# Performance work log

Measured on AMD Instinct MI355X. Metric: run time of the kernel, lower is better.

Reference implementation:

```python
import jax, jax.numpy as jnp
import numpy as np

NUM_EMBEDDINGS = 2048
EMBEDDING_DIM = 128
BETA = 0.25


def setup_inputs() -> dict:
    key = jax.random.key(0)
    k1, k2 = jax.random.split(key)
    z = jax.random.normal(k1, (64, 32, 32, EMBEDDING_DIM), dtype=jnp.float32)
    # nn.Embedding init: uniform(-1/K, 1/K)
    emb = jax.random.uniform(k2, (NUM_EMBEDDINGS, EMBEDDING_DIM), dtype=jnp.float32,
                             minval=-1.0 / NUM_EMBEDDINGS, maxval=1.0 / NUM_EMBEDDINGS)
    return {"z": z, "emb": emb}


def reference(z, emb):
    beta = BETA
    flat = z.reshape(-1, EMBEDDING_DIM)  # [N, D]
    dist = (jnp.sum(flat * flat, axis=1, keepdims=True)
            - 2.0 * flat @ emb.T
            + jnp.sum(emb * emb, axis=1))
    indices = jnp.argmin(dist, axis=1)  # [N]
    quantized = emb[indices].reshape(z.shape)
    # commitment / codebook loss
    loss = (jnp.mean((jax.lax.stop_gradient(quantized) - z) ** 2)
            + beta * jnp.mean((quantized - jax.lax.stop_gradient(z)) ** 2))
    # straight-through estimator
    quantized_st = z + jax.lax.stop_gradient(quantized - z)
    indices_out = indices.reshape(z.shape[0], -1)
    return quantized_st, indices_out, loss
```

## Files before the change

### kernel.cpp

```cpp
#include <hip/hip_runtime.h>

#define NUM_EMB 2048
#define DIM     128
#define NVEC    65536
#define MARGIN  1.0e-3f
#define CAP     32
#define CHUNK   256
#define NCHUNK  (NUM_EMB / CHUNK)
#define ES      136
#define ZS      132

typedef float  f32x4 __attribute__((ext_vector_type(4)));
typedef short  s16x8 __attribute__((ext_vector_type(8)));

__device__ __forceinline__ ushort f2bf(float f) {
    unsigned u = __float_as_uint(f);
    u = (u + 0x7fffu + ((u >> 16) & 1u)) >> 16;
    return (ushort)u;
}

__device__ __forceinline__ float np_pairwise_sumsq_128(const float* __restrict__ p)
{
    float r[8];
    #pragma unroll
    for (int j = 0; j < 8; ++j) { float v = p[j]; r[j] = __fmul_rn(v, v); }
    #pragma unroll
    for (int i = 8; i < 128; i += 8)
        #pragma unroll
        for (int j = 0; j < 8; ++j) { float v = p[i + j]; r[j] = __fadd_rn(r[j], __fmul_rn(v, v)); }
    float s01 = __fadd_rn(r[0], r[1]);
    float s23 = __fadd_rn(r[2], r[3]);
    float s45 = __fadd_rn(r[4], r[5]);
    float s67 = __fadd_rn(r[6], r[7]);
    return __fadd_rn(__fadd_rn(s01, s23), __fadd_rn(s45, s67));
}

__device__ __forceinline__ float dot_seg(const float4* __restrict__ zp,
                                         const float4* __restrict__ ep,
                                         int seg, float dot)
{
    float4 e[8], zz[8];
    #pragma unroll
    for (int i = 0; i < 8; ++i) { e[i] = ep[seg * 8 + i]; zz[i] = zp[seg * 8 + i]; }
    #pragma unroll
    for (int i = 0; i < 8; ++i) {
        dot = fmaf(zz[i].x, e[i].x, dot);
        dot = fmaf(zz[i].y, e[i].y, dot);
        dot = fmaf(zz[i].z, e[i].z, dot);
        dot = fmaf(zz[i].w, e[i].w, dot);
    }
    return dot;
}

__global__ __launch_bounds__(256)
void prep_kernel(const float* __restrict__ emb,
                 float* __restrict__ enorm,
                 float* __restrict__ accum,
                 unsigned* __restrict__ cand_cnt,
                 ushort* __restrict__ emb_bf)
{
    int g = blockIdx.x * 256 + threadIdx.x;
    cand_cnt[g] = 0u;
    if (g == 0) *accum = 0.0f;

    float4 v = ((const float4*)emb)[g];
    ushort4 b;
    b.x = f2bf(v.x); b.y = f2bf(v.y); b.z = f2bf(v.z); b.w = f2bf(v.w);
    ((ushort4*)emb_bf)[g] = b;

    if (g < NUM_EMB)
        enorm[g] = np_pairwise_sumsq_128(emb + (size_t)g * DIM);
}

__global__ __launch_bounds__(256, 2)
void approx_kernel(const float* __restrict__ z,
                   const ushort* __restrict__ emb_bf,
                   const float* __restrict__ enorm,
                   unsigned* __restrict__ cand_cnt,
                   ushort* __restrict__ cand)
{
    __shared__ __align__(16) ushort eS[CHUNK * ES];
    __shared__ float cS[CHUNK];

    const int tid  = threadIdx.x;
    const int w    = tid >> 6;
    const int lane = tid & 63;
    const int col  = lane & 15;
    const int quad = lane >> 4;
    const int rowbase = blockIdx.x * 128 + w * 32;

    s16x8 afrag[2][4];
    #pragma unroll
    for (int rt = 0; rt < 2; ++rt) {
        const float* zr = z + (size_t)(rowbase + rt * 16 + col) * DIM;
        #pragma unroll
        for (int kt = 0; kt < 4; ++kt) {
            const float4* p = (const float4*)(zr + kt * 32 + quad * 8);
            float4 f0 = p[0], f1 = p[1];
            s16x8 a;
            a[0] = (short)f2bf(f0.x); a[1] = (short)f2bf(f0.y);
            a[2] = (short)f2bf(f0.z); a[3] = (short)f2bf(f0.w);
            a[4] = (short)f2bf(f1.x); a[5] = (short)f2bf(f1.y);
            a[6] = (short)f2bf(f1.z); a[7] = (short)f2bf(f1.w);
            afrag[rt][kt] = a;
        }
    }

    float minv[2][4], thr[2][4];
    #pragma unroll
    for (int rt = 0; rt < 2; ++rt)
        #pragma unroll
        for (int r = 0; r < 4; ++r) minv[rt][r] = 3.0e38f;

    for (int vis = 0; vis < 9; ++vis) {
        const int c = (vis == 0) ? 0 : (vis - 1);
        __syncthreads();
        const uint4* src = (const uint4*)(emb_bf + (size_t)c * CHUNK * DIM);
        #pragma unroll
        for (int i = 0; i < 16; ++i) {
            int li   = i * 256 + tid;
            int code = li >> 4, fc = li & 15;
            *(uint4*)&eS[code * ES + fc * 8] = src[li];
        }
        cS[tid] = enorm[c * CHUNK + tid];
        __syncthreads();

        #pragma unroll 4
        for (int t = 0; t < 16; ++t) {
            s16x8 bfrag[4];
            #pragma unroll
            for (int kt = 0; kt < 4; ++kt)
                bfrag[kt] = *(const s16x8*)&eS[(t * 16 + col) * ES + kt * 32 + quad * 8];

            f32x4 acc[2];
            #pragma unroll
            for (int rt = 0; rt < 2; ++rt) {
                f32x4 a = {0.0f, 0.0f, 0.0f, 0.0f};
                #pragma unroll
                for (int kt = 0; kt < 4; ++kt)
                    a = __builtin_amdgcn_mfma_f32_16x16x32_bf16(afrag[rt][kt], bfrag[kt], a, 0, 0, 0);
                acc[rt] = a;
            }

            float Cc     = cS[t * 16 + col];
            int   code_g = c * CHUNK + t * 16 + col;
            #pragma unroll
            for (int rt = 0; rt < 2; ++rt)
                #pragma unroll
                for (int r = 0; r < 4; ++r) {
                    float g = fmaf(-2.0f, acc[rt][r], Cc);
                    minv[rt][r] = fminf(minv[rt][r], g);
                    if (vis > 0 && g <= thr[rt][r]) {
                        int row_g = rowbase + rt * 16 + quad * 4 + r;
                        unsigned pos = atomicAdd(&cand_cnt[row_g], 1u);
                        if (pos < CAP) cand[(size_t)row_g * CAP + pos] = (ushort)code_g;
                    }
                }
        }

        #pragma unroll
        for (int rt = 0; rt < 2; ++rt)
            #pragma unroll
            for (int r = 0; r < 4; ++r) {
                float v = minv[rt][r];
                v = fminf(v, __shfl_xor(v, 1, 64));
                v = fminf(v, __shfl_xor(v, 2, 64));
                v = fminf(v, __shfl_xor(v, 4, 64));
                v = fminf(v, __shfl_xor(v, 8, 64));
                minv[rt][r] = v;
                thr[rt][r]  = v + MARGIN;
            }
    }
}

__global__ __launch_bounds__(256)
void rerank_kernel(const float* __restrict__ z,
                   const float* __restrict__ emb,
                   const float* __restrict__ enorm,
                   const unsigned* __restrict__ cand_cnt,
                   const ushort* __restrict__ cand,
                   float* __restrict__ out_q,
                   float* __restrict__ out_idx_f,
                   float* __restrict__ accum)
{
    __shared__ float zs[64 * ZS];
    __shared__ float As[64];
    __shared__ int   bidx[64];
    __shared__ int   ovf_list[64];
    __shared__ int   ovf_n;
    __shared__ float rv[4];
    __shared__ int   rvi[4];
    __shared__ float wsum[4];

    const int tid = threadIdx.x;
    const int m0  = blockIdx.x * 64;
    if (tid == 0) ovf_n = 0;

    #pragma unroll
    for (int i = 0; i < 8; ++i) {
        int li = tid + i * 256;
        int m  = li >> 5, dc = li & 31;
        float4 v = ((const float4*)(z + (size_t)(m0 + m) * DIM))[dc];
        *(float4*)&zs[m * ZS + dc * 4] = v;
    }
    __syncthreads();
    if (tid < 64) As[tid] = np_pairwise_sumsq_128(&zs[tid * ZS]);
    __syncthreads();

    const int row_l = tid >> 2;
    const int sub   = tid & 3;
    const int row_g = m0 + row_l;
    const unsigned cnt = cand_cnt[row_g];
    const float A = As[row_l];
    const float4* zp = (const float4*)&zs[row_l * ZS];

    float bv = 3.0e38f;
    int   bi = 0x7fffffff;

    if (cnt <= CAP) {
        for (unsigned ci = sub; ci < cnt; ci += 4) {
            int j = (int)cand[(size_t)row_g * CAP + ci];
            const float4* ep = (const float4*)(emb + (size_t)j * DIM);
            float dot = 0.0f;
            #pragma unroll
            for (int seg = 0; seg < 4; ++seg) dot = dot_seg(zp, ep, seg, dot);
            float t1 = fmaf(-2.0f, dot, A);
            float s  = __fadd_rn(t1, enorm[j]);
            if (s < bv || (s == bv && j < bi)) { bv = s; bi = j; }
        }
    }
    #pragma unroll
    for (int off = 1; off <= 2; off <<= 1) {
        float v  = __shfl_xor(bv, off, 64);
        int   ix = __shfl_xor(bi, off, 64);
        if (v < bv || (v == bv && ix < bi)) { bv = v; bi = ix; }
    }
    if (sub == 0) {
        if (cnt <= CAP) bidx[row_l] = bi;
        else { int p = atomicAdd(&ovf_n, 1); ovf_list[p] = row_l; }
    }
    __syncthreads();

    const int n_ovf = ovf_n;
    for (int o = 0; o < n_ovf; ++o) {
        const int rl = ovf_list[o];
        const float Ar = As[rl];
        const float4* zp2 = (const float4*)&zs[rl * ZS];
        float bv2 = 3.0e38f;
        int   bi2 = 0x7fffffff;
        for (int jj = 0; jj < 8; ++jj) {
            int j = tid * 8 + jj;
            const float4* ep = (const float4*)(emb + (size_t)j * DIM);
            float dot = 0.0f;
            #pragma unroll
            for (int seg = 0; seg < 4; ++seg) dot = dot_seg(zp2, ep, seg, dot);
            float t1 = fmaf(-2.0f, dot, Ar);
            float s  = __fadd_rn(t1, enorm[j]);
            if (s < bv2) { bv2 = s; bi2 = j; }
        }
        #pragma unroll
        for (int off = 1; off < 64; off <<= 1) {
            float v  = __shfl_xor(bv2, off, 64);
            int   ix = __shfl_xor(bi2, off, 64);
            if (v < bv2 || (v == bv2 && ix < bi2)) { bv2 = v; bi2 = ix; }
        }
        if ((tid & 63) == 0) { rv[tid >> 6] = bv2; rvi[tid >> 6] = bi2; }
        __syncthreads();
        if (tid == 0) {
            float fv = rv[0]; int fi = rvi[0];
            #pragma unroll
            for (int ww = 1; ww < 4; ++ww) {
                if (rv[ww] < fv || (rv[ww] == fv && rvi[ww] < fi)) { fv = rv[ww]; fi = rvi[ww]; }
            }
            bidx[rl] = fi;
        }
        __syncthreads();
    }

    if (tid < 64) out_idx_f[m0 + tid] = (float)bidx[tid];

    float part = 0.0f;
    #pragma unroll
    for (int i = 0; i < 8; ++i) {
        int li = tid + i * 256;
        int m  = li >> 5, dc = li & 31;
        int j  = bidx[m];
        float4 q  = ((const float4*)(emb + (size_t)j * DIM))[dc];
        float4 zv = *(const float4*)&zs[m * ZS + dc * 4];
        float4 o;
        o.x = __fadd_rn(zv.x, __fsub_rn(q.x, zv.x));
        o.y = __fadd_rn(zv.y, __fsub_rn(q.y, zv.y));
        o.z = __fadd_rn(zv.z, __fsub_rn(q.z, zv.z));
        o.w = __fadd_rn(zv.w, __fsub_rn(q.w, zv.w));
        ((float4*)out_q)[(size_t)(m0 + m) * 32 + dc] = o;
        float dx = q.x - zv.x, dy = q.y - zv.y, dz = q.z - zv.z, dw = q.w - zv.w;
        part += dx * dx + dy * dy + dz * dz + dw * dw;
    }
    #pragma unroll
    for (int off = 32; off > 0; off >>= 1)
        part += __shfl_down(part, off, 64);
    if ((tid & 63) == 0) wsum[tid >> 6] = part;
    __syncthreads();
    if (tid == 0) atomicAdd(accum, wsum[0] + wsum[1] + wsum[2] + wsum[3]);
}

__global__ void finalize_kernel(const float* __restrict__ accum,
                                float* __restrict__ out_loss)
{
    *out_loss = 1.25f * (*accum) / 8388608.0f;
}

extern "C" void kernel_launch(void* const* d_in, const int* in_sizes, int n_in,
                              void* d_out, int out_size, void* d_ws, size_t ws_size,
                              hipStream_t stream)
{
    const float* z   = (const float*)d_in[0];
    const float* emb = (const float*)d_in[1];
    float* out = (float*)d_out;

    char*     ws       = (char*)d_ws;
    float*    enorm    = (float*)ws;
    float*    accum    = (float*)(ws + 8192);
    unsigned* cand_cnt = (unsigned*)(ws + 16384);
    ushort*   cand     = (ushort*)(ws + 16384 + 262144);
    ushort*   emb_bf   = (ushort*)(ws + 16384 + 262144 + 4194304);

    prep_kernel   <<<NVEC / 256, 256, 0, stream>>>(emb, enorm, accum, cand_cnt, emb_bf);
    approx_kernel <<<512,        256, 0, stream>>>(z, emb_bf, enorm, cand_cnt, cand);
    rerank_kernel <<<NVEC / 64,  256, 0, stream>>>(z, emb, enorm, cand_cnt, cand,
                                                   out, out + 8388608, accum);
    finalize_kernel<<<1, 1, 0, stream>>>(accum, out + 8388608 + 65536);
}
```

Measured before the change: 275.7 us.

## Use 1024-thread approx blocks with one 16-row tile per wave

The approximate-distance kernel now runs 256 blocks of 16 waves instead of 512 blocks of 4 waves, and each wave owns 16 query rows rather than 32. The staged bf16 codebook chunk in shared memory is reused by four times as many waves, so L2-to-LDS traffic per query row drops. The cost is half as much MFMA work per B-fragment LDS read in each wave, which puts more pressure on LDS bandwidth, plus coarser blocks and heavier barrier synchronization.

Result: faster. 225.7 us (-18.1%).

```diff
diff --git a/kernel.cpp b/kernel.cpp
--- a/kernel.cpp
+++ b/kernel.cpp
@@ -72,7 +72,7 @@
         enorm[g] = np_pairwise_sumsq_128(emb + (size_t)g * DIM);
 }
 
-__global__ __launch_bounds__(256, 2)
+__global__ __launch_bounds__(1024, 1)
 void approx_kernel(const float* __restrict__ z,
                    const ushort* __restrict__ emb_bf,
                    const float* __restrict__ enorm,
@@ -87,12 +87,11 @@
     const int lane = tid & 63;
     const int col  = lane & 15;
     const int quad = lane >> 4;
-    const int rowbase = blockIdx.x * 128 + w * 32;
-
-    s16x8 afrag[2][4];
-    #pragma unroll
-    for (int rt = 0; rt < 2; ++rt) {
-        const float* zr = z + (size_t)(rowbase + rt * 16 + col) * DIM;
+    const int rowbase = blockIdx.x * 256 + w * 16;
+
+    s16x8 afrag[4];
+    {
+        const float* zr = z + (size_t)(rowbase + col) * DIM;
         #pragma unroll
         for (int kt = 0; kt < 4; ++kt) {
             const float4* p = (const float4*)(zr + kt * 32 + quad * 8);
@@ -102,27 +101,25 @@
             a[2] = (short)f2bf(f0.z); a[3] = (short)f2bf(f0.w);
             a[4] = (short)f2bf(f1.x); a[5] = (short)f2bf(f1.y);
             a[6] = (short)f2bf(f1.z); a[7] = (short)f2bf(f1.w);
-            afrag[rt][kt] = a;
-        }
-    }
-
-    float minv[2][4], thr[2][4];
-    #pragma unroll
-    for (int rt = 0; rt < 2; ++rt)
-        #pragma unroll
-        for (int r = 0; r < 4; ++r) minv[rt][r] = 3.0e38f;
+            afrag[kt] = a;
+        }
+    }
+
+    float minv[4], thr[4];
+    #pragma unroll
+    for (int r = 0; r < 4; ++r) minv[r] = 3.0e38f;
 
     for (int vis = 0; vis < 9; ++vis) {
         const int c = (vis == 0) ? 0 : (vis - 1);
         __syncthreads();
         const uint4* src = (const uint4*)(emb_bf + (size_t)c * CHUNK * DIM);
         #pragma unroll
-        for (int i = 0; i < 16; ++i) {
-            int li   = i * 256 + tid;
+        for (int i = 0; i < 4; ++i) {
+            int li   = i * 1024 + tid;
             int code = li >> 4, fc = li & 15;
             *(uint4*)&eS[code * ES + fc * 8] = src[li];
         }
-        cS[tid] = enorm[c * CHUNK + tid];
+        if (tid < CHUNK) cS[tid] = enorm[c * CHUNK + tid];
         __syncthreads();
 
         #pragma unroll 4
@@ -132,44 +129,35 @@
             for (int kt = 0; kt < 4; ++kt)
                 bfrag[kt] = *(const s16x8*)&eS[(t * 16 + col) * ES + kt * 32 + quad * 8];
 
-            f32x4 acc[2];
-            #pragma unroll
-            for (int rt = 0; rt < 2; ++rt) {
-                f32x4 a = {0.0f, 0.0f, 0.0f, 0.0f};
-                #pragma unroll
-                for (int kt = 0; kt < 4; ++kt)
-                    a = __builtin_amdgcn_mfma_f32_16x16x32_bf16(afrag[rt][kt], bfrag[kt], a, 0, 0, 0);
-                acc[rt] = a;
-            }
+            f32x4 a = {0.0f, 0.0f, 0.0f, 0.0f};
+            #pragma unroll
+            for (int kt = 0; kt < 4; ++kt)
+                a = __builtin_amdgcn_mfma_f32_16x16x32_bf16(afrag[kt], bfrag[kt], a, 0, 0, 0);
 
             float Cc     = cS[t * 16 + col];
             int   code_g = c * CHUNK + t * 16 + col;
             #pragma unroll
-            for (int rt = 0; rt < 2; ++rt)
-                #pragma unroll
-                for (int r = 0; r < 4; ++r) {
-                    float g = fmaf(-2.0f, acc[rt][r], Cc);
-                    minv[rt][r] = fminf(minv[rt][r], g);
-                    if (vis > 0 && g <= thr[rt][r]) {
-                        int row_g = rowbase + rt * 16 + quad * 4 + r;
-                        unsigned pos = atomicAdd(&cand_cnt[row_g], 1u);
-                        if (pos < CAP) cand[(size_t)row_g * CAP + pos] = (ushort)code_g;
-                    }
+            for (int r = 0; r < 4; ++r) {
+                float g = fmaf(-2.0f, a[r], Cc);
+                minv[r] = fminf(minv[r], g);
+                if (vis > 0 && g <= thr[r]) {
+                    int row_g = rowbase + quad * 4 + r;
+                    unsigned pos = atomicAdd(&cand_cnt[row_g], 1u);
+                    if (pos < CAP) cand[(size_t)row_g * CAP + pos] = (ushort)code_g;
                 }
-        }
-
-        #pragma unroll
-        for (int rt = 0; rt < 2; ++rt)
-            #pragma unroll
-            for (int r = 0; r < 4; ++r) {
-                float v = minv[rt][r];
-                v = fminf(v, __shfl_xor(v, 1, 64));
-                v = fminf(v, __shfl_xor(v, 2, 64));
-                v = fminf(v, __shfl_xor(v, 4, 64));
-                v = fminf(v, __shfl_xor(v, 8, 64));
-                minv[rt][r] = v;
-                thr[rt][r]  = v + MARGIN;
             }
+        }
+
+        #pragma unroll
+        for (int r = 0; r < 4; ++r) {
+            float v = minv[r];
+            v = fminf(v, __shfl_xor(v, 1, 64));
+            v = fminf(v, __shfl_xor(v, 2, 64));
+            v = fminf(v, __shfl_xor(v, 4, 64));
+            v = fminf(v, __shfl_xor(v, 8, 64));
+            minv[r] = v;
+            thr[r]  = v + MARGIN;
+        }
     }
 }
 
@@ -325,9 +313,9 @@
     ushort*   cand     = (ushort*)(ws + 16384 + 262144);
     ushort*   emb_bf   = (ushort*)(ws + 16384 + 262144 + 4194304);
 
-    prep_kernel   <<<NVEC / 256, 256, 0, stream>>>(emb, enorm, accum, cand_cnt, emb_bf);
-    approx_kernel <<<512,        256, 0, stream>>>(z, emb_bf, enorm, cand_cnt, cand);
-    rerank_kernel <<<NVEC / 64,  256, 0, stream>>>(z, emb, enorm, cand_cnt, cand,
-                                                   out, out + 8388608, accum);
+    prep_kernel   <<<NVEC / 256, 256,  0, stream>>>(emb, enorm, accum, cand_cnt, emb_bf);
+    approx_kernel <<<256,        1024, 0, stream>>>(z, emb_bf, enorm, cand_cnt, cand);
+    rerank_kernel <<<NVEC / 64,  256,  0, stream>>>(z, emb, enorm, cand_cnt, cand,
+                                                    out, out + 8388608, accum);
     finalize_kernel<<<1, 1, 0, stream>>>(accum, out + 8388608 + 65536);
 }
```
